# Performance work log

Measured on AMD Instinct MI355X. Metric: run time of the kernel, lower is better.

## Reference

```python
import jax, jax.numpy as jnp
import numpy as np

N_NODE, N_POD, N_SVC = 500, 20000, 2000
T, F, H, O = 16, 64, 128, 64


def _gconv(x, src, dst, n_dst, W, b):
    # DGL GraphConv, norm='both': out-deg^-1/2 on src, sum-aggregate, in-deg^-1/2 on dst, then linear.
    n_src = x.shape[0]
    outd = jnp.clip(jax.ops.segment_sum(jnp.ones(src.shape, x.dtype), src, num_segments=n_src), 1.0)
    ind = jnp.clip(jax.ops.segment_sum(jnp.ones(dst.shape, x.dtype), dst, num_segments=n_dst), 1.0)
    h = x * jax.lax.rsqrt(outd)[:, None, None]          # [n_src, T, F]
    m = jax.ops.segment_sum(h[src], dst, num_segments=n_dst)  # [n_dst, T, F]
    m = m * jax.lax.rsqrt(ind)[:, None, None]
    return jnp.einsum('ntf,fh->nth', m, W) + b


def _lstm_layer(x, Wih, Whh, bih, bhh):
    # PyTorch LSTM layer, gate order i,f,g,o; x: [B, T, I] batch_first.
    B = x.shape[0]
    Hh = Whh.shape[1]
    def step(carry, xt):
        h, c = carry
        g = xt @ Wih.T + h @ Whh.T + (bih + bhh)
        i, f, gg, o = jnp.split(g, 4, axis=-1)
        c = jax.nn.sigmoid(f) * c + jax.nn.sigmoid(i) * jnp.tanh(gg)
        h = jax.nn.sigmoid(o) * jnp.tanh(c)
        return (h, c), h
    init = (jnp.zeros((B, Hh), x.dtype), jnp.zeros((B, Hh), x.dtype))
    _, hs = jax.lax.scan(step, init, jnp.swapaxes(x, 0, 1))
    return jnp.swapaxes(hs, 0, 1)


def setup_inputs() -> dict:
    key = jax.random.key(0)
    ks = jax.random.split(key, 32)
    p = lambda k, shape, fan: (jax.random.normal(k, shape, jnp.float32) / np.sqrt(fan)).astype(jnp.float32)
    d = {
        'x_node': jax.random.normal(ks[0], (N_NODE, T, F), jnp.float32),
        'x_pod': jax.random.normal(ks[1], (N_POD, T, F), jnp.float32),
        'x_svc': jax.random.normal(ks[2], (N_SVC, T, F), jnp.float32),
        'sc_src': jax.random.randint(ks[3], (16000,), 0, N_SVC),
        'sc_dst': jax.random.randint(ks[4], (16000,), 0, N_SVC),
        'in_src': jax.random.randint(ks[5], (20000,), 0, N_POD),
        'in_dst': jax.random.randint(ks[6], (20000,), 0, N_NODE),
        'ni_src': jax.random.randint(ks[7], (20000,), 0, N_NODE),
        'ni_dst': jax.random.randint(ks[8], (20000,), 0, N_POD),
        'ii_src': jax.random.randint(ks[9], (100000,), 0, N_POD),
        'ii_dst': jax.random.randint(ks[10], (100000,), 0, N_POD),
        'si_src': jax.random.randint(ks[11], (20000,), 0, N_SVC),
        'si_dst': jax.random.randint(ks[12], (20000,), 0, N_POD),
        'is_src': jax.random.randint(ks[13], (20000,), 0, N_POD),
        'is_dst': jax.random.randint(ks[14], (20000,), 0, N_SVC),
        # GraphConv params: weight [in, out], bias [out]
        'W_sc': p(ks[15], (F, H), F), 'b_sc': jnp.zeros((H,), jnp.float32),
        'W_in': p(ks[16], (F, H), F), 'b_in': jnp.zeros((H,), jnp.float32),
        'W_ni': p(ks[17], (F, H), F), 'b_ni': jnp.zeros((H,), jnp.float32),
        'W_ii': p(ks[18], (F, H), F), 'b_ii': jnp.zeros((H,), jnp.float32),
        'W_si': p(ks[19], (F, H), F), 'b_si': jnp.zeros((H,), jnp.float32),
        'W_is': p(ks[20], (F, H), F), 'b_is': jnp.zeros((H,), jnp.float32),
        # 2-layer LSTM params
        'Wih0': p(ks[21], (4 * O, H), H), 'Whh0': p(ks[22], (4 * O, O), O),
        'bih0': jnp.zeros((4 * O,), jnp.float32), 'bhh0': jnp.zeros((4 * O,), jnp.float32),
        'Wih1': p(ks[23], (4 * O, O), O), 'Whh1': p(ks[24], (4 * O, O), O),
        'bih1': jnp.zeros((4 * O,), jnp.float32), 'bhh1': jnp.zeros((4 * O,), jnp.float32),
    }
    return d


def reference(x_node, x_pod, x_svc,
              sc_src, sc_dst, in_src, in_dst, ni_src, ni_dst,
              ii_src, ii_dst, si_src, si_dst, is_src, is_dst,
              W_sc, b_sc, W_in, b_in, W_ni, b_ni, W_ii, b_ii, W_si, b_si, W_is, b_is,
              Wih0, Whh0, bih0, bhh0, Wih1, Whh1, bih1, bhh1):
    # HeteroGraphConv with aggregate='mean' over edge types per dst node type,
    # vectorized over all T timesteps at once (the torch code loops per timestep).
    node = _gconv(x_pod, in_src, in_dst, N_NODE, W_in, b_in)  # only relation into 'node'
    pod = (_gconv(x_node, ni_src, ni_dst, N_POD, W_ni, b_ni)
           + _gconv(x_pod, ii_src, ii_dst, N_POD, W_ii, b_ii)
           + _gconv(x_svc, si_src, si_dst, N_POD, W_si, b_si)) / 3.0
    svc = (_gconv(x_svc, sc_src, sc_dst, N_SVC, W_sc, b_sc)
           + _gconv(x_pod, is_src, is_dst, N_SVC, W_is, b_is)) / 2.0
    feat = jax.nn.relu(jnp.concatenate([node, pod, svc], axis=0))  # [N_total, T, H]
    h = _lstm_layer(feat, Wih0, Whh0, bih0, bhh0)
    h = _lstm_layer(h, Wih1, Whh1, bih1, bhh1)
    return feat, jax.nn.relu(h)
```

## Files before the change

kernel.cpp:

```cpp
#include <hip/hip_runtime.h>

typedef unsigned int u32;

#define N_NODE_ 500
#define N_POD_  20000
#define N_SVC_  2000
#define N_TOT_  22500
#define T_ 16
#define F_ 64
#define H_ 128
#define O_ 64

#define OF_OUTD_SC  0
#define OF_IND_SC   2000
#define OF_OUTD_IN  4000
#define OF_IND_IN   24000
#define OF_OUTD_NI  24500
#define OF_IND_NI   25000
#define OF_OUTD_II  45000
#define OF_IND_II   65000
#define OF_OUTD_SI  85000
#define OF_IND_SI   87000
#define OF_OUTD_IS  107000
#define OF_IND_IS   127000
#define OF_DEG_END  129000
#define OF_W0       129024
#define OF_W1       (129024 + 49152)
#define G_F_SIZE    (129024 + 81920)
#define OI_CNT_IN 0
#define OI_CNT_NI 500
#define OI_CNT_II 20500
#define OI_CNT_SI 40500
#define OI_CNT_SC 60500
#define OI_CNT_IS 62500
#define OI_CNT_END 64500
#define OI_OFF_IN 64500
#define OI_OFF_NI 65001
#define OI_OFF_II 85002
#define OI_OFF_SI 105003
#define OI_OFF_SC 125004
#define OI_OFF_IS 127005
#define OI_CSR_IN 129006
#define OI_CSR_NI 149006
#define OI_CSR_II 169006
#define OI_CSR_SI 269006
#define OI_CSR_SC 289006
#define OI_CSR_IS 305006
#define G_I_SIZE  325006

__device__ __align__(16) float g_f[G_F_SIZE];
__device__ int g_i[G_I_SIZE];

__device__ __forceinline__ float sigf(float x) { return 1.0f / (1.0f + __expf(-x)); }

__global__ void zero_k() {
  int i = blockIdx.x * 256 + threadIdx.x;
  if (i < OF_DEG_END + 24) g_f[i] = 0.0f;
  if (i < OI_CNT_END) g_i[i] = 0;
}

__global__ void zero_cnt_k() {
  int i = blockIdx.x * 256 + threadIdx.x;
  if (i < OI_CNT_END) g_i[i] = 0;
}

__global__ void deg_cnt_k(const int* __restrict__ src, const int* __restrict__ dst, int n,
                          int o_outd, int o_ind, int o_cnt) {
  int e = blockIdx.x * 256 + threadIdx.x;
  if (e < n) {
    atomicAdd(&g_f[o_outd + src[e]], 1.0f);
    atomicAdd(&g_f[o_ind + dst[e]], 1.0f);
    atomicAdd(&g_i[o_cnt + dst[e]], 1);
  }
}

__global__ void rsqrt_deg_k() {
  int i = blockIdx.x * 256 + threadIdx.x;
  if (i < OF_DEG_END) g_f[i] = rsqrtf(fmaxf(g_f[i], 1.0f));
}

__global__ void transpose_w2_k(const float* __restrict__ in, int o_out, int K) {
  int i = blockIdx.x * 256 + threadIdx.x;
  if (i < 256 * K) {
    int r = i / K, k = i - r * K;
    int q = r >> 6, j = r & 63;
    g_f[o_out + k * 256 + (j << 2) + q] = in[i];
  }
}

__global__ void exscan6_k() {
  const int cnto[6] = {OI_CNT_IN, OI_CNT_NI, OI_CNT_II, OI_CNT_SI, OI_CNT_SC, OI_CNT_IS};
  const int offo[6] = {OI_OFF_IN, OI_OFF_NI, OI_OFF_II, OI_OFF_SI, OI_OFF_SC, OI_OFF_IS};
  const int ns[6] = {500, 20000, 20000, 20000, 2000, 2000};
  int rel = blockIdx.x;
  const int* cnt = g_i + cnto[rel];
  int* off = g_i + offo[rel];
  int n = ns[rel];
  __shared__ int base_s[257];
  __shared__ int part[256];
  int tid = threadIdx.x;
  int chunk = (n + 255) >> 8;
  int lo = tid * chunk;
  int hi = lo + chunk; if (hi > n) hi = n;
  int s = 0;
  for (int i = lo; i < hi; ++i) s += cnt[i];
  part[tid] = s;
  __syncthreads();
  if (tid == 0) {
    int run = 0;
    for (int j = 0; j < 256; ++j) { base_s[j] = run; run += part[j]; }
    base_s[256] = run;
  }
  __syncthreads();
  int run = base_s[tid];
  for (int i = lo; i < hi; ++i) { off[i] = run; run += cnt[i]; }
  if (tid == 0) off[n] = base_s[256];
}

__global__ void fill_csr_k(const int* __restrict__ src, const int* __restrict__ dst, int n,
                           int o_off, int o_cur, int o_csr) {
  int e = blockIdx.x * 256 + threadIdx.x;
  if (e < n) {
    int d = dst[e];
    int p = atomicAdd(&g_i[o_cur + d], 1);
    g_i[o_csr + g_i[o_off + d] + p] = src[e];
  }
}

template <int NREL>
__global__ __launch_bounds__(256) void gconv_gather_k(
    const float* __restrict__ x0, const float* __restrict__ x1, const float* __restrict__ x2,
    int off0, int off1, int off2, int csr0, int csr1, int csr2,
    int od0, int od1, int od2, int id0, int id1, int id2,
    const float* __restrict__ W0, const float* __restrict__ W1, const float* __restrict__ W2,
    const float* __restrict__ b0, const float* __restrict__ b1, const float* __restrict__ b2,
    float scale, float* __restrict__ outp) {
  const float* xs_[3] = {x0, x1, x2};
  const int offs[3] = {off0, off1, off2};
  const int csrs[3] = {csr0, csr1, csr2};
  const int ods[3] = {od0, od1, od2};
  const int ids[3] = {id0, id1, id2};
  const float* Ws[3] = {W0, W1, W2};
  const float* bs[3] = {b0, b1, b2};

  int node = blockIdx.x;
  int tid = threadIdx.x;
  int c = tid & 127;
  int rg = tid >> 7;
  __shared__ float msh[T_][F_];

  float bb = 0.0f;
#pragma unroll
  for (int rel = 0; rel < NREL; ++rel) bb += bs[rel][c];
  float acc[8];
#pragma unroll
  for (int i = 0; i < 8; ++i) acc[i] = bb;

#pragma unroll
  for (int rel = 0; rel < NREL; ++rel) {
    int e0 = g_i[offs[rel] + node], e1 = g_i[offs[rel] + node + 1];
    const int* csr = g_i + csrs[rel];
    const float* od = g_f + ods[rel];
    const float* xr = xs_[rel];
    float a0 = 0.0f, a1 = 0.0f, a2 = 0.0f, a3 = 0.0f;
    for (int e = e0; e < e1; ++e) {
      int s = csr[e];
      float rs = od[s];
      float4 v = ((const float4*)(xr + (size_t)s * 1024))[tid];
      a0 += v.x * rs;
      a1 += v.y * rs;
      a2 += v.z * rs;
      a3 += v.w * rs;
    }
    __syncthreads();
    float* mf = &msh[0][0];
    mf[tid * 4 + 0] = a0;
    mf[tid * 4 + 1] = a1;
    mf[tid * 4 + 2] = a2;
    mf[tid * 4 + 3] = a3;
    __syncthreads();
    float rind = g_f[ids[rel] + node];
    const float* W = Ws[rel];
#pragma unroll 4
    for (int f = 0; f < F_; ++f) {
      float w = W[f * H_ + c] * rind;
#pragma unroll
      for (int i = 0; i < 8; ++i) acc[i] += msh[rg * 8 + i][f] * w;
    }
  }
  float* o = outp + (size_t)node * (T_ * H_);
#pragma unroll
  for (int i = 0; i < 8; ++i) {
    float v = acc[i] * scale;
    o[(rg * 8 + i) * H_ + c] = fmaxf(v, 0.0f);
  }
}

#define RW 11

__device__ __forceinline__ void gemv_lds(float acc[RW][4], const float* xrow0,
                                         const float4* __restrict__ Wb, int nk4, int l) {
#pragma unroll 2
  for (int k4 = 0; k4 < nk4; ++k4) {
    const float4* wp = Wb + (k4 << 8) + l;
    float4 w0 = wp[0];
    float4 w1 = wp[64];
    float4 w2 = wp[128];
    float4 w3 = wp[192];
#pragma unroll
    for (int r = 0; r < RW; ++r) {
      float4 xv = *(const float4*)(xrow0 + r * 256 + k4 * 4);
      acc[r][0] += xv.x * w0.x; acc[r][1] += xv.x * w0.y; acc[r][2] += xv.x * w0.z; acc[r][3] += xv.x * w0.w;
      acc[r][0] += xv.y * w1.x; acc[r][1] += xv.y * w1.y; acc[r][2] += xv.y * w1.z; acc[r][3] += xv.y * w1.w;
      acc[r][0] += xv.z * w2.x; acc[r][1] += xv.z * w2.y; acc[r][2] += xv.z * w2.z; acc[r][3] += xv.z * w2.w;
      acc[r][0] += xv.w * w3.x; acc[r][1] += xv.w * w3.y; acc[r][2] += xv.w * w3.z; acc[r][3] += xv.w * w3.w;
    }
  }
}

__global__ __launch_bounds__(256, 2) void lstm_lds_k(
    const float* __restrict__ feat,
    const float* __restrict__ bih0, const float* __restrict__ bhh0,
    const float* __restrict__ bih1, const float* __restrict__ bhh1,
    float* __restrict__ out2) {
  const float4* W0v = (const float4*)(g_f + OF_W0);
  const float4* W1v = (const float4*)(g_f + OF_W1);
  __shared__ __align__(16) float xh[4][RW][256];
  int tid = threadIdx.x;
  int l = tid & 63;
  int wid = tid >> 6;
  int row0 = (blockIdx.x * 4 + wid) * RW;
  float* xw = &xh[wid][0][0];

  float bb0[4], bb1[4];
#pragma unroll
  for (int q = 0; q < 4; ++q) {
    bb0[q] = bih0[q * 64 + l] + bhh0[q * 64 + l];
    bb1[q] = bih1[q * 64 + l] + bhh1[q * 64 + l];
  }

  const float* xb[RW];
  bool vld[RW];
#pragma unroll
  for (int r = 0; r < RW; ++r) {
    int row = row0 + r;
    vld[r] = row < N_TOT_;
    xb[r] = feat + (size_t)(vld[r] ? row : 0) * (T_ * H_);
  }

  float c0[RW] = {}, c1[RW] = {};
#pragma unroll
  for (int r = 0; r < RW; ++r) {
    xw[r * 256 + 128 + l] = 0.0f;
    xw[r * 256 + 192 + l] = 0.0f;
  }

  for (int t = 0; t < T_; ++t) {
#pragma unroll
    for (int r = 0; r < RW; ++r) {
      xw[r * 256 + l] = xb[r][t * H_ + l];
      xw[r * 256 + 64 + l] = xb[r][t * H_ + 64 + l];
    }

    float acc[RW][4];
#pragma unroll
    for (int r = 0; r < RW; ++r)
#pragma unroll
      for (int q = 0; q < 4; ++q) acc[r][q] = bb0[q];

    gemv_lds(acc, xw, W0v, 48, l);

#pragma unroll
    for (int r = 0; r < RW; ++r) {
      float iv = sigf(acc[r][0]);
      float fv = sigf(acc[r][1]);
      float gv = tanhf(acc[r][2]);
      float ov = sigf(acc[r][3]);
      float cc = fv * c0[r] + iv * gv;
      c0[r] = cc;
      xw[r * 256 + 128 + l] = ov * tanhf(cc);
    }

#pragma unroll
    for (int r = 0; r < RW; ++r)
#pragma unroll
      for (int q = 0; q < 4; ++q) acc[r][q] = bb1[q];

    gemv_lds(acc, xw + 128, W1v, 32, l);

#pragma unroll
    for (int r = 0; r < RW; ++r) {
      float iv = sigf(acc[r][0]);
      float fv = sigf(acc[r][1]);
      float gv = tanhf(acc[r][2]);
      float ov = sigf(acc[r][3]);
      float cc = fv * c1[r] + iv * gv;
      c1[r] = cc;
      float hh = ov * tanhf(cc);
      xw[r * 256 + 192 + l] = hh;
      if (vld[r]) out2[((size_t)(row0 + r) * T_ + t) * O_ + l] = fmaxf(hh, 0.0f);
    }
  }
}

extern "C" void kernel_launch(void* const* d_in, const int* in_sizes, int n_in,
                              void* d_out, int out_size, void* d_ws, size_t ws_size,
                              hipStream_t stream) {
  (void)in_sizes; (void)n_in; (void)out_size; (void)d_ws; (void)ws_size;
  const float* x_node = (const float*)d_in[0];
  const float* x_pod  = (const float*)d_in[1];
  const float* x_svc  = (const float*)d_in[2];
  const int* sc_src = (const int*)d_in[3];
  const int* sc_dst = (const int*)d_in[4];
  const int* in_src = (const int*)d_in[5];
  const int* in_dst = (const int*)d_in[6];
  const int* ni_src = (const int*)d_in[7];
  const int* ni_dst = (const int*)d_in[8];
  const int* ii_src = (const int*)d_in[9];
  const int* ii_dst = (const int*)d_in[10];
  const int* si_src = (const int*)d_in[11];
  const int* si_dst = (const int*)d_in[12];
  const int* is_src = (const int*)d_in[13];
  const int* is_dst = (const int*)d_in[14];
  const float* W_sc = (const float*)d_in[15]; const float* b_sc = (const float*)d_in[16];
  const float* W_in = (const float*)d_in[17]; const float* b_in = (const float*)d_in[18];
  const float* W_ni = (const float*)d_in[19]; const float* b_ni = (const float*)d_in[20];
  const float* W_ii = (const float*)d_in[21]; const float* b_ii = (const float*)d_in[22];
  const float* W_si = (const float*)d_in[23]; const float* b_si = (const float*)d_in[24];
  const float* W_is = (const float*)d_in[25]; const float* b_is = (const float*)d_in[26];
  const float* Wih0 = (const float*)d_in[27]; const float* Whh0 = (const float*)d_in[28];
  const float* bih0 = (const float*)d_in[29]; const float* bhh0 = (const float*)d_in[30];
  const float* Wih1 = (const float*)d_in[31]; const float* Whh1 = (const float*)d_in[32];
  const float* bih1 = (const float*)d_in[33]; const float* bhh1 = (const float*)d_in[34];

  float* out_feat = (float*)d_out;
  float* out_h = out_feat + (size_t)N_TOT_ * T_ * H_;

  zero_k<<<(OF_DEG_END + 24 + 255) / 256, 256, 0, stream>>>();

  deg_cnt_k<<<(16000 + 255) / 256, 256, 0, stream>>>(sc_src, sc_dst, 16000, OF_OUTD_SC, OF_IND_SC, OI_CNT_SC);
  deg_cnt_k<<<(20000 + 255) / 256, 256, 0, stream>>>(in_src, in_dst, 20000, OF_OUTD_IN, OF_IND_IN, OI_CNT_IN);
  deg_cnt_k<<<(20000 + 255) / 256, 256, 0, stream>>>(ni_src, ni_dst, 20000, OF_OUTD_NI, OF_IND_NI, OI_CNT_NI);
  deg_cnt_k<<<(100000 + 255) / 256, 256, 0, stream>>>(ii_src, ii_dst, 100000, OF_OUTD_II, OF_IND_II, OI_CNT_II);
  deg_cnt_k<<<(20000 + 255) / 256, 256, 0, stream>>>(si_src, si_dst, 20000, OF_OUTD_SI, OF_IND_SI, OI_CNT_SI);
  deg_cnt_k<<<(20000 + 255) / 256, 256, 0, stream>>>(is_src, is_dst, 20000, OF_OUTD_IS, OF_IND_IS, OI_CNT_IS);
  rsqrt_deg_k<<<(OF_DEG_END + 255) / 256, 256, 0, stream>>>();

  transpose_w2_k<<<(256 * 128 + 255) / 256, 256, 0, stream>>>(Wih0, OF_W0, 128);
  transpose_w2_k<<<(256 * 64 + 255) / 256, 256, 0, stream>>>(Whh0, OF_W0 + 128 * 256, 64);
  transpose_w2_k<<<(256 * 64 + 255) / 256, 256, 0, stream>>>(Wih1, OF_W1, 64);
  transpose_w2_k<<<(256 * 64 + 255) / 256, 256, 0, stream>>>(Whh1, OF_W1 + 64 * 256, 64);

  exscan6_k<<<6, 256, 0, stream>>>();
  zero_cnt_k<<<(OI_CNT_END + 255) / 256, 256, 0, stream>>>();
  fill_csr_k<<<(20000 + 255) / 256, 256, 0, stream>>>(in_src, in_dst, 20000, OI_OFF_IN, OI_CNT_IN, OI_CSR_IN);
  fill_csr_k<<<(20000 + 255) / 256, 256, 0, stream>>>(ni_src, ni_dst, 20000, OI_OFF_NI, OI_CNT_NI, OI_CSR_NI);
  fill_csr_k<<<(100000 + 255) / 256, 256, 0, stream>>>(ii_src, ii_dst, 100000, OI_OFF_II, OI_CNT_II, OI_CSR_II);
  fill_csr_k<<<(20000 + 255) / 256, 256, 0, stream>>>(si_src, si_dst, 20000, OI_OFF_SI, OI_CNT_SI, OI_CSR_SI);
  fill_csr_k<<<(16000 + 255) / 256, 256, 0, stream>>>(sc_src, sc_dst, 16000, OI_OFF_SC, OI_CNT_SC, OI_CSR_SC);
  fill_csr_k<<<(20000 + 255) / 256, 256, 0, stream>>>(is_src, is_dst, 20000, OI_OFF_IS, OI_CNT_IS, OI_CSR_IS);

  gconv_gather_k<1><<<N_NODE_, 256, 0, stream>>>(
      x_pod, nullptr, nullptr, OI_OFF_IN, 0, 0, OI_CSR_IN, 0, 0,
      OF_OUTD_IN, 0, 0, OF_IND_IN, 0, 0,
      W_in, nullptr, nullptr, b_in, nullptr, nullptr, 1.0f, out_feat);
  gconv_gather_k<3><<<N_POD_, 256, 0, stream>>>(
      x_node, x_pod, x_svc, OI_OFF_NI, OI_OFF_II, OI_OFF_SI, OI_CSR_NI, OI_CSR_II, OI_CSR_SI,
      OF_OUTD_NI, OF_OUTD_II, OF_OUTD_SI, OF_IND_NI, OF_IND_II, OF_IND_SI,
      W_ni, W_ii, W_si, b_ni, b_ii, b_si, 1.0f / 3.0f,
      out_feat + (size_t)N_NODE_ * (T_ * H_));
  gconv_gather_k<2><<<N_SVC_, 256, 0, stream>>>(
      x_svc, x_pod, nullptr, OI_OFF_SC, OI_OFF_IS, 0, OI_CSR_SC, OI_CSR_IS, 0,
      OF_OUTD_SC, OF_OUTD_IS, 0, OF_IND_SC, OF_IND_IS, 0,
      W_sc, W_is, nullptr, b_sc, b_is, nullptr, 0.5f,
      out_feat + (size_t)(N_NODE_ + N_POD_) * (T_ * H_));

  lstm_lds_k<<<512, 256, 0, stream>>>(
      out_feat, bih0, bhh0, bih1, bhh1, out_h);
}
```

Baseline: 1.653 ms.

## Batch graph prep launches, raise LSTM occupancy, prefetch inputs, use fast tanh

Replaces the per-relation degree-count and CSR-fill launches with single 2D-grid kernels, and merges the rsqrt-degree and weight-transpose steps into one kernel. Count zeroing moves into the exclusive scan. The LSTM kernel now processes 6 rows per wave instead of 11, with launch bounds for 4 blocks per CU and twice the grid. It prefetches the next timestep's input into registers and uses an exp-based tanh. These changes target launch overhead, LSTM latency hiding and transcendental cost; in exchange, weight reuse per row drops and there is slight precision risk from the fast tanh.

```diff
diff --git a/kernel.cpp b/kernel.cpp
--- a/kernel.cpp
+++ b/kernel.cpp
@@ -53,39 +53,69 @@
 
 __device__ __forceinline__ float sigf(float x) { return 1.0f / (1.0f + __expf(-x)); }
 
+__device__ __forceinline__ float tanhf_fast(float x) {
+  float ax = fabsf(x);
+  float e = __expf(2.0f * ax);
+  float t = 1.0f - 2.0f / (e + 1.0f);
+  return copysignf(t, x);
+}
+
 __global__ void zero_k() {
   int i = blockIdx.x * 256 + threadIdx.x;
   if (i < OF_DEG_END + 24) g_f[i] = 0.0f;
   if (i < OI_CNT_END) g_i[i] = 0;
 }
 
-__global__ void zero_cnt_k() {
+struct Rels {
+  const int* src[6];
+  const int* dst[6];
+  int n[6];
+  int o_outd[6];
+  int o_ind[6];
+  int o_cnt[6];
+  int o_off[6];
+  int o_csr[6];
+};
+
+__global__ void deg_all_k(Rels R) {
+  int rel = blockIdx.y;
+  int e = blockIdx.x * 256 + threadIdx.x;
+  if (e < R.n[rel]) {
+    atomicAdd(&g_f[R.o_outd[rel] + R.src[rel][e]], 1.0f);
+    atomicAdd(&g_f[R.o_ind[rel] + R.dst[rel][e]], 1.0f);
+    atomicAdd(&g_i[R.o_cnt[rel] + R.dst[rel][e]], 1);
+  }
+}
+
+__global__ void fill_all_k(Rels R) {
+  int rel = blockIdx.y;
+  int e = blockIdx.x * 256 + threadIdx.x;
+  if (e < R.n[rel]) {
+    int d = R.dst[rel][e];
+    int p = atomicAdd(&g_i[R.o_cnt[rel] + d], 1);
+    g_i[R.o_csr[rel] + g_i[R.o_off[rel] + d] + p] = R.src[rel][e];
+  }
+}
+
+__device__ __forceinline__ void tw_one(const float* __restrict__ in, int o_out, int K, int idx) {
+  int r = idx / K, k = idx - r * K;
+  int q = r >> 6, j = r & 63;
+  g_f[o_out + k * 256 + (j << 2) + q] = in[idx];
+}
+
+#define PREP2_TOT (OF_DEG_END + 32768 + 16384 + 16384 + 16384)
+__global__ void prep2_k(const float* __restrict__ Wih0, const float* __restrict__ Whh0,
+                        const float* __restrict__ Wih1, const float* __restrict__ Whh1) {
   int i = blockIdx.x * 256 + threadIdx.x;
-  if (i < OI_CNT_END) g_i[i] = 0;
-}
-
-__global__ void deg_cnt_k(const int* __restrict__ src, const int* __restrict__ dst, int n,
-                          int o_outd, int o_ind, int o_cnt) {
-  int e = blockIdx.x * 256 + threadIdx.x;
-  if (e < n) {
-    atomicAdd(&g_f[o_outd + src[e]], 1.0f);
-    atomicAdd(&g_f[o_ind + dst[e]], 1.0f);
-    atomicAdd(&g_i[o_cnt + dst[e]], 1);
-  }
-}
-
-__global__ void rsqrt_deg_k() {
-  int i = blockIdx.x * 256 + threadIdx.x;
-  if (i < OF_DEG_END) g_f[i] = rsqrtf(fmaxf(g_f[i], 1.0f));
-}
-
-__global__ void transpose_w2_k(const float* __restrict__ in, int o_out, int K) {
-  int i = blockIdx.x * 256 + threadIdx.x;
-  if (i < 256 * K) {
-    int r = i / K, k = i - r * K;
-    int q = r >> 6, j = r & 63;
-    g_f[o_out + k * 256 + (j << 2) + q] = in[i];
-  }
+  if (i < OF_DEG_END) { g_f[i] = rsqrtf(fmaxf(g_f[i], 1.0f)); return; }
+  int j = i - OF_DEG_END;
+  if (j < 32768) { tw_one(Wih0, OF_W0, 128, j); return; }
+  j -= 32768;
+  if (j < 16384) { tw_one(Whh0, OF_W0 + 32768, 64, j); return; }
+  j -= 16384;
+  if (j < 16384) { tw_one(Wih1, OF_W1, 64, j); return; }
+  j -= 16384;
+  if (j < 16384) { tw_one(Whh1, OF_W1 + 16384, 64, j); return; }
 }
 
 __global__ void exscan6_k() {
@@ -93,7 +123,7 @@
   const int offo[6] = {OI_OFF_IN, OI_OFF_NI, OI_OFF_II, OI_OFF_SI, OI_OFF_SC, OI_OFF_IS};
   const int ns[6] = {500, 20000, 20000, 20000, 2000, 2000};
   int rel = blockIdx.x;
-  const int* cnt = g_i + cnto[rel];
+  int* cnt = g_i + cnto[rel];
   int* off = g_i + offo[rel];
   int n = ns[rel];
   __shared__ int base_s[257];
@@ -113,18 +143,8 @@
   }
   __syncthreads();
   int run = base_s[tid];
-  for (int i = lo; i < hi; ++i) { off[i] = run; run += cnt[i]; }
+  for (int i = lo; i < hi; ++i) { off[i] = run; run += cnt[i]; cnt[i] = 0; }
   if (tid == 0) off[n] = base_s[256];
-}
-
-__global__ void fill_csr_k(const int* __restrict__ src, const int* __restrict__ dst, int n,
-                           int o_off, int o_cur, int o_csr) {
-  int e = blockIdx.x * 256 + threadIdx.x;
-  if (e < n) {
-    int d = dst[e];
-    int p = atomicAdd(&g_i[o_cur + d], 1);
-    g_i[o_csr + g_i[o_off + d] + p] = src[e];
-  }
 }
 
 template <int NREL>
@@ -196,7 +216,7 @@
   }
 }
 
-#define RW 11
+#define RW 6
 
 __device__ __forceinline__ void gemv_lds(float acc[RW][4], const float* xrow0,
                                          const float4* __restrict__ Wb, int nk4, int l) {
@@ -218,7 +238,7 @@
   }
 }
 
-__global__ __launch_bounds__(256, 2) void lstm_lds_k(
+__global__ __launch_bounds__(256, 4) void lstm_lds_k(
     const float* __restrict__ feat,
     const float* __restrict__ bih0, const float* __restrict__ bhh0,
     const float* __restrict__ bih1, const float* __restrict__ bhh1,
@@ -255,11 +275,24 @@
     xw[r * 256 + 192 + l] = 0.0f;
   }
 
+  float xn0[RW], xn1[RW];
+#pragma unroll
+  for (int r = 0; r < RW; ++r) {
+    xn0[r] = xb[r][l];
+    xn1[r] = xb[r][64 + l];
+  }
+
   for (int t = 0; t < T_; ++t) {
 #pragma unroll
     for (int r = 0; r < RW; ++r) {
-      xw[r * 256 + l] = xb[r][t * H_ + l];
-      xw[r * 256 + 64 + l] = xb[r][t * H_ + 64 + l];
+      xw[r * 256 + l] = xn0[r];
+      xw[r * 256 + 64 + l] = xn1[r];
+    }
+    int tn = (t + 1) & 15;
+#pragma unroll
+    for (int r = 0; r < RW; ++r) {
+      xn0[r] = xb[r][tn * H_ + l];
+      xn1[r] = xb[r][tn * H_ + 64 + l];
     }
 
     float acc[RW][4];
@@ -274,11 +307,11 @@
     for (int r = 0; r < RW; ++r) {
       float iv = sigf(acc[r][0]);
       float fv = sigf(acc[r][1]);
-      float gv = tanhf(acc[r][2]);
+      float gv = tanhf_fast(acc[r][2]);
       float ov = sigf(acc[r][3]);
       float cc = fv * c0[r] + iv * gv;
       c0[r] = cc;
-      xw[r * 256 + 128 + l] = ov * tanhf(cc);
+      xw[r * 256 + 128 + l] = ov * tanhf_fast(cc);
     }
 
 #pragma unroll
@@ -292,11 +325,11 @@
     for (int r = 0; r < RW; ++r) {
       float iv = sigf(acc[r][0]);
       float fv = sigf(acc[r][1]);
-      float gv = tanhf(acc[r][2]);
+      float gv = tanhf_fast(acc[r][2]);
       float ov = sigf(acc[r][3]);
       float cc = fv * c1[r] + iv * gv;
       c1[r] = cc;
-      float hh = ov * tanhf(cc);
+      float hh = ov * tanhf_fast(cc);
       xw[r * 256 + 192 + l] = hh;
       if (vld[r]) out2[((size_t)(row0 + r) * T_ + t) * O_ + l] = fmaxf(hh, 0.0f);
     }
@@ -336,29 +369,34 @@
   float* out_feat = (float*)d_out;
   float* out_h = out_feat + (size_t)N_TOT_ * T_ * H_;
 
+  Rels R;
+  R.src[0] = in_src; R.dst[0] = in_dst; R.n[0] = 20000;
+  R.o_outd[0] = OF_OUTD_IN; R.o_ind[0] = OF_IND_IN; R.o_cnt[0] = OI_CNT_IN;
+  R.o_off[0] = OI_OFF_IN; R.o_csr[0] = OI_CSR_IN;
+  R.src[1] = ni_src; R.dst[1] = ni_dst; R.n[1] = 20000;
+  R.o_outd[1] = OF_OUTD_NI; R.o_ind[1] = OF_IND_NI; R.o_cnt[1] = OI_CNT_NI;
+  R.o_off[1] = OI_OFF_NI; R.o_csr[1] = OI_CSR_NI;
+  R.src[2] = ii_src; R.dst[2] = ii_dst; R.n[2] = 100000;
+  R.o_outd[2] = OF_OUTD_II; R.o_ind[2] = OF_IND_II; R.o_cnt[2] = OI_CNT_II;
+  R.o_off[2] = OI_OFF_II; R.o_csr[2] = OI_CSR_II;
+  R.src[3] = si_src; R.dst[3] = si_dst; R.n[3] = 20000;
+  R.o_outd[3] = OF_OUTD_SI; R.o_ind[3] = OF_IND_SI; R.o_cnt[3] = OI_CNT_SI;
+  R.o_off[3] = OI_OFF_SI; R.o_csr[3] = OI_CSR_SI;
+  R.src[4] = sc_src; R.dst[4] = sc_dst; R.n[4] = 16000;
+  R.o_outd[4] = OF_OUTD_SC; R.o_ind[4] = OF_IND_SC; R.o_cnt[4] = OI_CNT_SC;
+  R.o_off[4] = OI_OFF_SC; R.o_csr[4] = OI_CSR_SC;
+  R.src[5] = is_src; R.dst[5] = is_dst; R.n[5] = 20000;
+  R.o_outd[5] = OF_OUTD_IS; R.o_ind[5] = OF_IND_IS; R.o_cnt[5] = OI_CNT_IS;
+  R.o_off[5] = OI_OFF_IS; R.o_csr[5] = OI_CSR_IS;
+
   zero_k<<<(OF_DEG_END + 24 + 255) / 256, 256, 0, stream>>>();
 
-  deg_cnt_k<<<(16000 + 255) / 256, 256, 0, stream>>>(sc_src, sc_dst, 16000, OF_OUTD_SC, OF_IND_SC, OI_CNT_SC);
-  deg_cnt_k<<<(20000 + 255) / 256, 256, 0, stream>>>(in_src, in_dst, 20000, OF_OUTD_IN, OF_IND_IN, OI_CNT_IN);
-  deg_cnt_k<<<(20000 + 255) / 256, 256, 0, stream>>>(ni_src, ni_dst, 20000, OF_OUTD_NI, OF_IND_NI, OI_CNT_NI);
-  deg_cnt_k<<<(100000 + 255) / 256, 256, 0, stream>>>(ii_src, ii_dst, 100000, OF_OUTD_II, OF_IND_II, OI_CNT_II);
-  deg_cnt_k<<<(20000 + 255) / 256, 256, 0, stream>>>(si_src, si_dst, 20000, OF_OUTD_SI, OF_IND_SI, OI_CNT_SI);
-  deg_cnt_k<<<(20000 + 255) / 256, 256, 0, stream>>>(is_src, is_dst, 20000, OF_OUTD_IS, OF_IND_IS, OI_CNT_IS);
-  rsqrt_deg_k<<<(OF_DEG_END + 255) / 256, 256, 0, stream>>>();
-
-  transpose_w2_k<<<(256 * 128 + 255) / 256, 256, 0, stream>>>(Wih0, OF_W0, 128);
-  transpose_w2_k<<<(256 * 64 + 255) / 256, 256, 0, stream>>>(Whh0, OF_W0 + 128 * 256, 64);
-  transpose_w2_k<<<(256 * 64 + 255) / 256, 256, 0, stream>>>(Wih1, OF_W1, 64);
-  transpose_w2_k<<<(256 * 64 + 255) / 256, 256, 0, stream>>>(Whh1, OF_W1 + 64 * 256, 64);
+  deg_all_k<<<dim3((100000 + 255) / 256, 6), 256, 0, stream>>>(R);
+
+  prep2_k<<<(PREP2_TOT + 255) / 256, 256, 0, stream>>>(Wih0, Whh0, Wih1, Whh1);
 
   exscan6_k<<<6, 256, 0, stream>>>();
-  zero_cnt_k<<<(OI_CNT_END + 255) / 256, 256, 0, stream>>>();
-  fill_csr_k<<<(20000 + 255) / 256, 256, 0, stream>>>(in_src, in_dst, 20000, OI_OFF_IN, OI_CNT_IN, OI_CSR_IN);
-  fill_csr_k<<<(20000 + 255) / 256, 256, 0, stream>>>(ni_src, ni_dst, 20000, OI_OFF_NI, OI_CNT_NI, OI_CSR_NI);
-  fill_csr_k<<<(100000 + 255) / 256, 256, 0, stream>>>(ii_src, ii_dst, 100000, OI_OFF_II, OI_CNT_II, OI_CSR_II);
-  fill_csr_k<<<(20000 + 255) / 256, 256, 0, stream>>>(si_src, si_dst, 20000, OI_OFF_SI, OI_CNT_SI, OI_CSR_SI);
-  fill_csr_k<<<(16000 + 255) / 256, 256, 0, stream>>>(sc_src, sc_dst, 16000, OI_OFF_SC, OI_CNT_SC, OI_CSR_SC);
-  fill_csr_k<<<(20000 + 255) / 256, 256, 0, stream>>>(is_src, is_dst, 20000, OI_OFF_IS, OI_CNT_IS, OI_CSR_IS);
+  fill_all_k<<<dim3((100000 + 255) / 256, 6), 256, 0, stream>>>(R);
 
   gconv_gather_k<1><<<N_NODE_, 256, 0, stream>>>(
       x_pod, nullptr, nullptr, OI_OFF_IN, 0, 0, OI_CSR_IN, 0, 0,
@@ -375,6 +413,6 @@
       W_sc, W_is, nullptr, b_sc, b_is, nullptr, 0.5f,
       out_feat + (size_t)(N_NODE_ + N_POD_) * (T_ * H_));
 
-  lstm_lds_k<<<512, 256, 0, stream>>>(
+  lstm_lds_k<<<1024, 256, 0, stream>>>(
       out_feat, bih0, bhh0, bih1, bhh1, out_h);
 }
```

Result: slower. 1.907 ms (+15.3%).
